# Kernel tuning notes

Hardware: AMD Instinct MI355X
Metric: run time of the kernel (lower is better)

The kernel has to match this reference:

```python
import jax, jax.numpy as jnp
import numpy as np

DIM = 128
HEADS = 8
DIM_HEAD = 128  # must equal DIM for the module's shapes to be consistent
INNER = HEADS * DIM_HEAD  # 1024
B, N = 16, 2048
SCALE = 1.0 / (DIM // 2 + 1)  # 1/65


def setup_inputs() -> dict:
    key = jax.random.key(0)
    k1, k2, k3 = jax.random.split(key, 3)
    x = jax.random.normal(k1, (B, N, DIM), dtype=jnp.float32)
    w_qkv = jax.random.normal(k2, (DIM, 3 * INNER), dtype=jnp.float32) * (DIM ** -0.5)
    w_out = jax.random.normal(k3, (INNER, DIM), dtype=jnp.float32) * (INNER ** -0.5)
    b_out = jnp.zeros((DIM,), dtype=jnp.float32)
    return {"x": x, "w_qkv": w_qkv, "w_out": w_out, "b_out": b_out}


def reference(x, w_qkv, w_out, b_out):
    b, n, dim = x.shape
    qkv = x @ w_qkv                                   # [b, n, 3*inner]
    q, k, v = jnp.split(qkv, 3, axis=-1)
    # b n (h d) -> b h n d
    to_heads = lambda t: t.reshape(b, n, HEADS, DIM_HEAD).transpose(0, 2, 1, 3)
    q, k, v = to_heads(q), to_heads(k), to_heads(v)
    xq_ft = jnp.abs(jnp.fft.rfft(q * SCALE, axis=-1))  # [b, h, n, f] real
    xk_ft = jnp.abs(jnp.fft.rfft(k * SCALE, axis=-1))
    xv_ft = jnp.fft.rfft(v, axis=-1)                   # complex
    att = jnp.einsum('bhex,bhey->bhxy', xq_ft, xk_ft)  # [b, h, f, f]
    att = jax.nn.softmax(att, axis=-1)
    xqkv_ft = jnp.einsum('bhxy,bhey->bhex', att.astype(xv_ft.dtype), xv_ft)
    out = jnp.fft.irfft(xqkv_ft, n=dim, axis=-1)       # [b, h, n, dim]
    out = out.transpose(0, 2, 1, 3).reshape(b, n, HEADS * dim)  # b n (h d)
    return out @ w_out + b_out
```

## Files before the change

kernel.cpp:

```cpp
#include <hip/hip_runtime.h>
#include <hip/hip_bf16.h>
#include <math.h>

#define NB    16
#define NSEQ  2048
#define MROWS (NB*NSEQ)

typedef __attribute__((ext_vector_type(8))) short bf16x8;
typedef __attribute__((ext_vector_type(4))) float f32x4;

__device__ __forceinline__ void g2l16(const void* g, void* l) {
    __builtin_amdgcn_global_load_lds(
        (const __attribute__((address_space(1))) void*)g,
        (__attribute__((address_space(3))) void*)l, 16, 0, 0);
}

__device__ __forceinline__ ushort f2bfu(float x) {
    __hip_bfloat16 t = __float2bfloat16(x);
    return *reinterpret_cast<ushort*>(&t);
}

__global__ __launch_bounds__(256) void k_misc(const float* __restrict__ x,
                                              const float* __restrict__ wqkv,
                                              const float* __restrict__ wout,
                                              __hip_bfloat16* __restrict__ Xb,
                                              ushort* __restrict__ Wvb,
                                              ushort* __restrict__ Wqkb,
                                              ushort* __restrict__ Gcat,
                                              ushort* __restrict__ Fcs,
                                              ushort* __restrict__ Bas) {
    __shared__ float tc[128], ts[128];
    int tid = threadIdx.x;
    int bid = blockIdx.x;
    if (bid < 4096) {
        int i = bid * 256 + tid;
        float4 v = ((const float4*)x)[i];
        __hip_bfloat16 o[4] = {__float2bfloat16(v.x), __float2bfloat16(v.y),
                               __float2bfloat16(v.z), __float2bfloat16(v.w)};
        *(ushort4*)((ushort*)Xb + (size_t)i * 4) = *(const ushort4*)o;
    } else if (bid < 4224) {
        int u = bid - 4096;
        float4 v = *(const float4*)(wqkv + (size_t)u * 3072 + 2048 + tid * 4);
        ushort o[4] = {f2bfu(v.x), f2bfu(v.y), f2bfu(v.z), f2bfu(v.w)};
        *(ushort4*)(Wvb + (size_t)u * 1024 + tid * 4) = *(const ushort4*)o;
    } else if (bid < 4352) {
        int u = bid - 4224;
        #pragma unroll
        for (int it = 0; it < 2; ++it) {
            int i = it * 256 + tid;
            float4 v = ((const float4*)(wqkv + (size_t)u * 3072))[i];
            ushort o[4] = {f2bfu(v.x), f2bfu(v.y), f2bfu(v.z), f2bfu(v.w)};
            *(ushort4*)(Wqkb + (size_t)u * 2048 + i * 4) = *(const ushort4*)o;
        }
    } else if (bid < 4872) {
        int hx = bid - 4352;
        if (tid < 128) {
            float a = (float)tid / 64.0f;
            tc[tid] = cospif(a);
            ts[tid] = sinpif(a);
        }
        __syncthreads();
        if (tid < 128) {
            int h = hx / 65, xx = hx - h * 65;
            float w = (xx == 0 || xx == 64) ? (1.0f / 128.0f) : (2.0f / 128.0f);
            float ar = 0.f, ai = 0.f;
            #pragma unroll 8
            for (int d = 0; d < 128; ++d) {
                float wv = wout[(size_t)(h * 128 + d) * 128 + tid];
                int m = (xx * d) & 127;
                ar = fmaf(wv, tc[m], ar);
                ai = fmaf(wv, ts[m], ai);
            }
            ushort* gp = Gcat + ((size_t)(h * 128 + tid)) * 160;
            gp[xx] = f2bfu(ar * w);
            gp[80 + xx] = f2bfu(-ai * w);
            if (xx == 0) {
                for (int k = 65; k < 80; ++k) gp[k] = 0;
                for (int k = 145; k < 160; ++k) gp[k] = 0;
            }
        }
    } else if (bid < 4888) {
        int r = (bid - 4872) * 16 + (tid >> 4);
        int d = r & 127;
        int y0 = (tid & 15) * 6;
        #pragma unroll
        for (int k = 0; k < 6; ++k) {
            int y = y0 + k;
            float v = 0.f;
            if (y < 65) {
                float a = (float)((d * y) & 127) / 64.0f;
                v = (r < 128) ? cospif(a) : -sinpif(a);
            }
            Fcs[r * 96 + y] = f2bfu(v);
        }
    } else {
        int idx = bid - 4888;
        int rj = idx * 16 + (tid >> 4);
        int ri = (rj >= 80) ? 1 : 0;
        int f = rj - ri * 80;
        int d0 = (tid & 15) * 8;
        #pragma unroll
        for (int k = 0; k < 8; ++k) {
            int d = d0 + k;
            float a = (float)((f * d) & 127) / 64.0f;
            float v = (ri ? -sinpif(a) : cospif(a)) * (1.0f / 65.0f);
            Bas[rj * 128 + d] = f2bfu(v);
        }
    }
}

__global__ __launch_bounds__(256) void k_wfold(const ushort* __restrict__ Wqkb,
                                               const ushort* __restrict__ Bas,
                                               ushort* __restrict__ Wt2) {
    __shared__ ushort As[64 * 128];
    __shared__ ushort Bs[160 * 128];
    int tid = threadIdx.x;
    int wave = tid >> 6, lane = tid & 63;
    int reg = blockIdx.x >> 4;
    int h = (blockIdx.x >> 1) & 7;
    int uh = blockIdx.x & 1;
    const ushort* ga = Wqkb + (size_t)(uh * 64) * 2048 + reg * 1024 + h * 128;
    #pragma unroll
    for (int it = 0; it < 4; ++it) {
        int q0 = wave * 256 + it * 64;
        int q = q0 + lane;
        int row = q >> 4, cp = q & 15;
        int gc = cp ^ (row & 15);
        g2l16(ga + (size_t)row * 2048 + gc * 8, As + q0 * 8);
    }
    #pragma unroll
    for (int it = 0; it < 10; ++it) {
        int q0 = it * 256 + wave * 64;
        int q = q0 + lane;
        int row = q >> 4, cp = q & 15;
        int gc = cp ^ (row & 15);
        g2l16(Bas + (size_t)row * 128 + gc * 8, Bs + q0 * 8);
    }
    __syncthreads();

    f32x4 acc[2][5];
    #pragma unroll
    for (int i = 0; i < 2; ++i)
        #pragma unroll
        for (int j = 0; j < 5; ++j) acc[i][j] = (f32x4){0.f, 0.f, 0.f, 0.f};

    int lr = lane & 15, lk = lane >> 4;
    int wr = (wave >> 1) * 32;
    int wn = (wave & 1) * 80;
    #pragma unroll
    for (int kk = 0; kk < 4; ++kk) {
        bf16x8 af[2], bfr[5];
        int c = kk * 4 + lk;
        #pragma unroll
        for (int i = 0; i < 2; ++i) {
            int m = wr + i * 16 + lr;
            af[i] = *(const bf16x8*)(As + m * 128 + (c ^ (m & 15)) * 8);
        }
        #pragma unroll
        for (int j = 0; j < 5; ++j) {
            int n = wn + j * 16 + lr;
            bfr[j] = *(const bf16x8*)(Bs + n * 128 + (c ^ (n & 15)) * 8);
        }
        #pragma unroll
        for (int i = 0; i < 2; ++i)
            #pragma unroll
            for (int j = 0; j < 5; ++j)
                acc[i][j] = __builtin_amdgcn_mfma_f32_16x16x32_bf16(af[i], bfr[j], acc[i][j], 0, 0, 0);
    }

    #pragma unroll
    for (int j = 0; j < 5; ++j) {
        int rj = wn + j * 16 + lr;
        int n = (h * 2 + reg) * 160 + rj;
        #pragma unroll
        for (int i = 0; i < 2; ++i) {
            int c0 = uh * 64 + wr + i * 16 + lk * 4;
            union { ushort4 u4; ushort u[4]; } pk;
            #pragma unroll
            for (int r = 0; r < 4; ++r) pk.u[r] = f2bfu(acc[i][j][r]);
            *(ushort4*)(Wt2 + (size_t)n * 128 + c0) = pk.u4;
        }
    }
}

__global__ __launch_bounds__(320, 3) void k_fuse(const __hip_bfloat16* __restrict__ Xb,
                                                 const ushort* __restrict__ Wt2,
                                                 float* __restrict__ attp) {
    __shared__ ushort As[128 * 128];
    __shared__ ushort S[160 * 128];
    int tid = threadIdx.x;
    int wave = tid >> 6, lane = tid & 63;
    int lr = lane & 15, lk = lane >> 4;
    int lin = blockIdx.y * 128 + blockIdx.x;
    int nl = (lin & 7) * 64 + (lin >> 3);
    int b = nl >> 5;
    int epart = (nl >> 3) & 3, h = nl & 7;
    size_t erow0 = (size_t)b * NSEQ + (size_t)epart * 512;
    const ushort* wh = Wt2 + (size_t)h * 320 * 128;

    bf16x8 bw[4][4];
    #pragma unroll
    for (int ks = 0; ks < 4; ++ks)
        #pragma unroll
        for (int rb = 0; rb < 4; ++rb) {
            int n = rb * 80 + wave * 16 + lr;
            bw[ks][rb] = *(const bf16x8*)(wh + (size_t)n * 128 + (ks * 4 + lk) * 8);
        }

    {
        const ushort* gx = (const ushort*)Xb + erow0 * 128;
        for (int r = wave; r < 32; r += 5) {
            int q0 = r * 64, q = q0 + lane;
            int row = q >> 4, cp = q & 15;
            int gc = cp ^ (row & 15);
            g2l16(gx + (size_t)row * 128 + gc * 8, As + q0 * 8);
        }
    }
    __syncthreads();

    f32x4 acc2[5];
    #pragma unroll
    for (int j = 0; j < 5; ++j) acc2[j] = (f32x4){0.f, 0.f, 0.f, 0.f};

    for (int it = 0; it < 4; ++it) {
        #pragma unroll
        for (int et = 0; et < 8; ++et) {
            f32x4 a4[4];
            #pragma unroll
            for (int rb = 0; rb < 4; ++rb) a4[rb] = (f32x4){0.f, 0.f, 0.f, 0.f};
            #pragma unroll
            for (int ks = 0; ks < 4; ++ks) {
                int m = et * 16 + lr;
                bf16x8 xa = *(const bf16x8*)(As + m * 128 + (((ks * 4 + lk) ^ (m & 15))) * 8);
                #pragma unroll
                for (int rb = 0; rb < 4; ++rb)
                    a4[rb] = __builtin_amdgcn_mfma_f32_16x16x32_bf16(xa, bw[ks][rb], a4[rb], 0, 0, 0);
            }
            int e4 = et * 16 + lk * 4;
            int cq = e4 >> 3, sub = e4 & 7;
            union { ushort4 u4; ushort u[4]; } pq, pk2;
            #pragma unroll
            for (int r = 0; r < 4; ++r) {
                pq.u[r]  = f2bfu(__builtin_amdgcn_sqrtf(a4[0][r] * a4[0][r] + a4[1][r] * a4[1][r]));
                pk2.u[r] = f2bfu(__builtin_amdgcn_sqrtf(a4[2][r] * a4[2][r] + a4[3][r] * a4[3][r]));
            }
            int fq = wave * 16 + lr;
            int fk = 80 + wave * 16 + lr;
            *(ushort4*)(S + fq * 128 + ((cq ^ (fq & 15)) << 3) + sub) = pq.u4;
            *(ushort4*)(S + fk * 128 + ((cq ^ (fk & 15)) << 3) + sub) = pk2.u4;
        }
        __syncthreads();
        if (it < 3) {
            const ushort* gx = (const ushort*)Xb + (erow0 + (size_t)(it + 1) * 128) * 128;
            for (int r = wave; r < 32; r += 5) {
                int q0 = r * 64, q = q0 + lane;
                int row = q >> 4, cp = q & 15;
                int gc = cp ^ (row & 15);
                g2l16(gx + (size_t)row * 128 + gc * 8, As + q0 * 8);
            }
        }
        #pragma unroll
        for (int ks = 0; ks < 4; ++ks) {
            int cg = ks * 4 + lk;
            int xr = wave * 16 + lr;
            bf16x8 qa = *(const bf16x8*)(S + xr * 128 + ((cg ^ (xr & 15)) << 3));
            #pragma unroll
            for (int kt = 0; kt < 5; ++kt) {
                int yr = 80 + kt * 16 + lr;
                bf16x8 kb = *(const bf16x8*)(S + yr * 128 + ((cg ^ (yr & 15)) << 3));
                acc2[kt] = __builtin_amdgcn_mfma_f32_16x16x32_bf16(qa, kb, acc2[kt], 0, 0, 0);
            }
        }
        __syncthreads();
    }

    float* outp = attp + ((size_t)(b * 8 + h) * 4 + epart) * 6400;
    #pragma unroll
    for (int kt = 0; kt < 5; ++kt)
        #pragma unroll
        for (int r = 0; r < 4; ++r)
            outp[(wave * 16 + lk * 4 + r) * 80 + kt * 16 + lr] = acc2[kt][r];
}

__global__ void k_softmax(const float* __restrict__ attp, ushort* __restrict__ AttB) {
    int xx = blockIdx.x;
    int bh = blockIdx.y;
    int lane = threadIdx.x;
    ushort* Ab = AttB + (size_t)bh * 8320;
    if (xx >= 65) {
        Ab[xx * 104 + lane] = 0;
        if (lane < 40) Ab[xx * 104 + 64 + lane] = 0;
        return;
    }
    const float* base = attp + (size_t)bh * 4 * 6400 + xx * 80;
    float v0 = 0.f, v1 = 0.f;
    #pragma unroll
    for (int c = 0; c < 4; ++c) {
        v0 += base[(size_t)c * 6400 + lane];
        if (lane == 0) v1 += base[(size_t)c * 6400 + 64];
    }
    float v1b = __shfl(v1, 0);
    float m = fmaxf(v0, v1b);
    #pragma unroll
    for (int off = 32; off >= 1; off >>= 1) m = fmaxf(m, __shfl_xor(m, off));
    float e0 = expf(v0 - m);
    float e1 = expf(v1b - m);
    float s = e0;
    #pragma unroll
    for (int off = 32; off >= 1; off >>= 1) s += __shfl_xor(s, off);
    s += e1;
    float inv = 1.0f / s;
    Ab[xx * 104 + lane] = f2bfu(e0 * inv);
    if (lane == 0) Ab[xx * 104 + 64] = f2bfu(e1 * inv);
    if (lane < 39) Ab[xx * 104 + 65 + lane] = 0;
}

__global__ __launch_bounds__(256) void k_TP(const ushort* __restrict__ AttB,
                                            const ushort* __restrict__ Fcs,
                                            const ushort* __restrict__ Gcat,
                                            ushort* __restrict__ Pt) {
    __shared__ ushort A3[128 * 168];
    int tid = threadIdx.x;
    int wave = tid >> 6, lane = tid & 63;
    int lr = lane & 15, quad = lane >> 4;
    int chalf = blockIdx.x, bh = blockIdx.y;
    int b = bh >> 3, h = bh & 7;

    uint2 z2; z2.x = 0; z2.y = 0;
    uint2* A3v = (uint2*)A3;
    #pragma unroll 4
    for (int i = tid; i < 128 * 168 / 4; i += 256) A3v[i] = z2;
    __syncthreads();
    const ushort* Ab = AttB + (size_t)bh * 8320;

    f32x4 acc1[4][5];
    #pragma unroll
    for (int i = 0; i < 4; ++i)
        #pragma unroll
        for (int j = 0; j < 5; ++j) acc1[i][j] = (f32x4){0.f, 0.f, 0.f, 0.f};
    #pragma unroll
    for (int ks = 0; ks < 3; ++ks) {
        bf16x8 af[4], bfr[5];
        #pragma unroll
        for (int mi = 0; mi < 4; ++mi)
            af[mi] = *(const bf16x8*)(Fcs + (size_t)((wave * 4 + mi) * 16 + lr) * 96 + ks * 32 + quad * 8);
        #pragma unroll
        for (int nt = 0; nt < 5; ++nt)
            bfr[nt] = *(const bf16x8*)(Ab + (nt * 16 + lr) * 104 + ks * 32 + quad * 8);
        #pragma unroll
        for (int mi = 0; mi < 4; ++mi)
            #pragma unroll
            for (int nt = 0; nt < 5; ++nt)
                acc1[mi][nt] = __builtin_amdgcn_mfma_f32_16x16x32_bf16(af[mi], bfr[nt], acc1[mi][nt], 0, 0, 0);
    }
    #pragma unroll
    for (int nt = 0; nt < 5; ++nt) {
        int x = nt * 16 + lr;
        if (x < 65) {
            #pragma unroll
            for (int mi = 0; mi < 4; ++mi) {
                int wbase = (wave * 4 + mi) * 16 + quad * 4;
                #pragma unroll
                for (int r = 0; r < 4; ++r) {
                    int which = wbase + r;
                    int d = which & 127;
                    int kc = (which >> 7) * 80 + x;
                    A3[d * 168 + kc] = f2bfu(acc1[mi][nt][r]);
                }
            }
        }
    }
    __syncthreads();

    f32x4 acc2[2][4];
    #pragma unroll
    for (int i = 0; i < 2; ++i)
        #pragma unroll
        for (int j = 0; j < 4; ++j) acc2[i][j] = (f32x4){0.f, 0.f, 0.f, 0.f};
    const ushort* Gh = Gcat + (size_t)h * 128 * 160;
    #pragma unroll
    for (int ks = 0; ks < 5; ++ks) {
        bf16x8 a2[2], b2[4];
        #pragma unroll
        for (int mi = 0; mi < 2; ++mi)
            a2[mi] = *(const bf16x8*)(A3 + ((wave * 2 + mi) * 16 + lr) * 168 + ks * 32 + quad * 8);
        #pragma unroll
        for (int nt = 0; nt < 4; ++nt)
            b2[nt] = *(const bf16x8*)(Gh + (size_t)(chalf * 64 + nt * 16 + lr) * 160 + ks * 32 + quad * 8);
        #pragma unroll
        for (int mi = 0; mi < 2; ++mi)
            #pragma unroll
            for (int nt = 0; nt < 4; ++nt)
                acc2[mi][nt] = __builtin_amdgcn_mfma_f32_16x16x32_bf16(a2[mi], b2[nt], acc2[mi][nt], 0, 0, 0);
    }
    #pragma unroll
    for (int mi = 0; mi < 2; ++mi) {
        int dbase = (wave * 2 + mi) * 16 + quad * 4;
        #pragma unroll
        for (int nt = 0; nt < 4; ++nt) {
            int c = chalf * 64 + nt * 16 + lr;
            union { ushort4 u4; ushort u[4]; } pk;
            #pragma unroll
            for (int r = 0; r < 4; ++r) pk.u[r] = f2bfu(acc2[mi][nt][r]);
            *(ushort4*)(Pt + ((size_t)(b * 128 + c)) * 1024 + h * 128 + dbase) = pk.u4;
        }
    }
}

__global__ __launch_bounds__(256) void k_R(const ushort* __restrict__ Wvb,
                                           const ushort* __restrict__ Pt,
                                           ushort* __restrict__ Rt) {
    __shared__ ushort As[64 * 128];
    __shared__ ushort Bs[64 * 128];
    int tid = threadIdx.x;
    int wave = tid >> 6, lane = tid & 63;
    int b = blockIdx.x >> 2;
    int nq = (blockIdx.x >> 1) & 1;
    int uq = blockIdx.x & 1;
    const ushort* pb = Pt + (size_t)b * 128 * 1024;

    f32x4 acc[2][2];
    #pragma unroll
    for (int i = 0; i < 2; ++i)
        #pragma unroll
        for (int j = 0; j < 2; ++j) acc[i][j] = (f32x4){0.f, 0.f, 0.f, 0.f};

    int lr = lane & 15, lk = lane >> 4;
    int wr = (wave >> 1) * 32, wc = (wave & 1) * 32;

    for (int k0 = 0; k0 < 1024; k0 += 128) {
        __syncthreads();
        #pragma unroll
        for (int it = 0; it < 4; ++it) {
            int q = wave * 256 + it * 64 + lane;
            int row = q >> 4, cp = q & 15;
            int gc = cp ^ (row & 15);
            int lbase = (wave * 256 + it * 64) * 8;
            g2l16(Wvb + (size_t)(uq * 64 + row) * 1024 + k0 + gc * 8, As + lbase);
            g2l16(pb + (size_t)(nq * 64 + row) * 1024 + k0 + gc * 8, Bs + lbase);
        }
        __syncthreads();
        #pragma unroll
        for (int kk = 0; kk < 4; ++kk) {
            bf16x8 af[2], bfr[2];
            int c = kk * 4 + lk;
            #pragma unroll
            for (int i = 0; i < 2; ++i) {
                int m = wr + i * 16 + lr;
                af[i] = *(const bf16x8*)(As + m * 128 + (c ^ (m & 15)) * 8);
                int n = wc + i * 16 + lr;
                bfr[i] = *(const bf16x8*)(Bs + n * 128 + (c ^ (n & 15)) * 8);
            }
            #pragma unroll
            for (int i = 0; i < 2; ++i)
                #pragma unroll
                for (int j = 0; j < 2; ++j)
                    acc[i][j] = __builtin_amdgcn_mfma_f32_16x16x32_bf16(af[i], bfr[j], acc[i][j], 0, 0, 0);
        }
    }
    #pragma unroll
    for (int i = 0; i < 2; ++i) {
        int ubase = uq * 64 + wr + i * 16 + lk * 4;
        #pragma unroll
        for (int j = 0; j < 2; ++j) {
            int n = nq * 64 + wc + j * 16 + lr;
            union { ushort4 u4; ushort u[4]; } pk;
            #pragma unroll
            for (int r = 0; r < 4; ++r) pk.u[r] = f2bfu(acc[i][j][r]);
            *(ushort4*)(Rt + (size_t)b * 16384 + n * 128 + ubase) = pk.u4;
        }
    }
}

__global__ __launch_bounds__(256) void k_out(const __hip_bfloat16* __restrict__ Xb,
                                             const ushort* __restrict__ Rt,
                                             const float* __restrict__ bout,
                                             float* __restrict__ out) {
    __shared__ ushort As[128 * 128];
    __shared__ ushort Bs[128 * 128];
    int tid = threadIdx.x;
    int wave = tid >> 6, lane = tid & 63;
    int m0 = blockIdx.x * 128;
    int b = blockIdx.x >> 4;
    const ushort* ga = (const ushort*)Xb + (size_t)m0 * 128;
    const ushort* gb = Rt + (size_t)b * 16384;
    #pragma unroll
    for (int it = 0; it < 8; ++it) {
        int q = wave * 512 + it * 64 + lane;
        int row = q >> 4, cp = q & 15;
        int gc = cp ^ (row & 15);
        int lbase = (wave * 512 + it * 64) * 8;
        g2l16(ga + (size_t)row * 128 + gc * 8, As + lbase);
        g2l16(gb + (size_t)row * 128 + gc * 8, Bs + lbase);
    }
    __syncthreads();

    f32x4 acc[4][4];
    #pragma unroll
    for (int i = 0; i < 4; ++i)
        #pragma unroll
        for (int j = 0; j < 4; ++j) acc[i][j] = (f32x4){0.f, 0.f, 0.f, 0.f};

    int lr = lane & 15, lk = lane >> 4;
    int wr = (wave >> 1) * 64, wc = (wave & 1) * 64;
    #pragma unroll
    for (int kk = 0; kk < 4; ++kk) {
        bf16x8 af[4], bfr[4];
        int c = kk * 4 + lk;
        #pragma unroll
        for (int i = 0; i < 4; ++i) {
            int m = wr + i * 16 + lr;
            af[i] = *(const bf16x8*)(As + m * 128 + (c ^ (m & 15)) * 8);
            int n = wc + i * 16 + lr;
            bfr[i] = *(const bf16x8*)(Bs + n * 128 + (c ^ (n & 15)) * 8);
        }
        #pragma unroll
        for (int i = 0; i < 4; ++i)
            #pragma unroll
            for (int j = 0; j < 4; ++j)
                acc[i][j] = __builtin_amdgcn_mfma_f32_16x16x32_bf16(af[i], bfr[j], acc[i][j], 0, 0, 0);
    }

    #pragma unroll
    for (int i = 0; i < 4; ++i) {
        int gr = m0 + wr + i * 16 + lk * 4;
        #pragma unroll
        for (int j = 0; j < 4; ++j) {
            int gcol = wc + j * 16 + lr;
            float bias = bout[gcol];
            #pragma unroll
            for (int r = 0; r < 4; ++r)
                out[(size_t)(gr + r) * 128 + gcol] = acc[i][j][r] + bias;
        }
    }
}

extern "C" void kernel_launch(void* const* d_in, const int* in_sizes, int n_in,
                              void* d_out, int out_size, void* d_ws, size_t ws_size,
                              hipStream_t stream) {
    const float* x    = (const float*)d_in[0];
    const float* wqkv = (const float*)d_in[1];
    const float* wout = (const float*)d_in[2];
    const float* bout = (const float*)d_in[3];
    float* out = (float*)d_out;

    char* ws = (char*)d_ws;
    size_t off = 0;
    auto alloc = [&](size_t bytes) -> void* {
        void* p = (void*)(ws + off);
        off += (bytes + 255) & ~(size_t)255;
        return p;
    };
    ushort* Wt2  = (ushort*)alloc((size_t)8 * 320 * 128 * 2);
    ushort* Gcat = (ushort*)alloc((size_t)8 * 128 * 160 * 2);
    ushort* Fcs  = (ushort*)alloc((size_t)256 * 96 * 2);
    ushort* Wvb  = (ushort*)alloc((size_t)128 * 1024 * 2);
    ushort* Wqkb = (ushort*)alloc((size_t)128 * 2048 * 2);
    ushort* Bas  = (ushort*)alloc((size_t)160 * 128 * 2);
    __hip_bfloat16* Xb = (__hip_bfloat16*)alloc((size_t)MROWS * 128 * 2);
    float* attp = (float*)alloc((size_t)128 * 4 * 6400 * 4);
    ushort* AttB = (ushort*)alloc((size_t)128 * 8320 * 2);
    ushort* Pt  = (ushort*)alloc((size_t)16 * 128 * 1024 * 2);
    ushort* Rt  = (ushort*)alloc((size_t)16 * 128 * 128 * 2);

    k_misc<<<dim3(4898), 256, 0, stream>>>(x, wqkv, wout, Xb, Wvb, Wqkb, Gcat, Fcs, Bas);
    k_wfold<<<dim3(32), 256, 0, stream>>>(Wqkb, Bas, Wt2);
    k_fuse<<<dim3(128, 4), 320, 0, stream>>>(Xb, Wt2, attp);
    k_softmax<<<dim3(80, 128), 64, 0, stream>>>(attp, AttB);
    k_TP<<<dim3(2, 128), 256, 0, stream>>>(AttB, Fcs, Gcat, Pt);
    k_R<<<dim3(64), 256, 0, stream>>>(Wvb, Pt, Rt);
    k_out<<<dim3(256), 256, 0, stream>>>(Xb, Rt, bout, out);
}
```

Measured before the change: 148.4 us.

## Split k_fuse work across 10 waves, halving per-wave Q/K and attention tiles

Doubles the k_fuse block from 5 to 10 waves. Each wave pair now splits the projection work: one wave computes the Q magnitude rows and the other the K magnitude rows. The attention-score tiles are split 3/2 between the two waves. This halves per-wave register use and MFMA chains so more waves can hide latency, at the cost of an uneven split in the attention phase and a lower blocks-per-CU bound.

```diff
diff --git a/kernel.cpp b/kernel.cpp
--- a/kernel.cpp
+++ b/kernel.cpp
@@ -183,7 +183,7 @@
     }
 }
 
-__global__ __launch_bounds__(320, 3) void k_fuse(const __hip_bfloat16* __restrict__ Xb,
+__global__ __launch_bounds__(640, 2) void k_fuse(const __hip_bfloat16* __restrict__ Xb,
                                                  const ushort* __restrict__ Wt2,
                                                  float* __restrict__ attp) {
     __shared__ ushort As[128 * 128];
@@ -191,6 +191,8 @@
     int tid = threadIdx.x;
     int wave = tid >> 6, lane = tid & 63;
     int lr = lane & 15, lk = lane >> 4;
+    int g = wave >> 1;
+    int half = wave & 1;
     int lin = blockIdx.y * 128 + blockIdx.x;
     int nl = (lin & 7) * 64 + (lin >> 3);
     int b = nl >> 5;
@@ -198,18 +200,18 @@
     size_t erow0 = (size_t)b * NSEQ + (size_t)epart * 512;
     const ushort* wh = Wt2 + (size_t)h * 320 * 128;
 
-    bf16x8 bw[4][4];
+    bf16x8 bw[4][2];
     #pragma unroll
     for (int ks = 0; ks < 4; ++ks)
         #pragma unroll
-        for (int rb = 0; rb < 4; ++rb) {
-            int n = rb * 80 + wave * 16 + lr;
-            bw[ks][rb] = *(const bf16x8*)(wh + (size_t)n * 128 + (ks * 4 + lk) * 8);
+        for (int j = 0; j < 2; ++j) {
+            int n = (half * 2 + j) * 80 + g * 16 + lr;
+            bw[ks][j] = *(const bf16x8*)(wh + (size_t)n * 128 + (ks * 4 + lk) * 8);
         }
 
     {
         const ushort* gx = (const ushort*)Xb + erow0 * 128;
-        for (int r = wave; r < 32; r += 5) {
+        for (int r = wave; r < 32; r += 10) {
             int q0 = r * 64, q = q0 + lane;
             int row = q >> 4, cp = q & 15;
             int gc = cp ^ (row & 15);
@@ -218,41 +220,40 @@
     }
     __syncthreads();
 
-    f32x4 acc2[5];
-    #pragma unroll
-    for (int j = 0; j < 5; ++j) acc2[j] = (f32x4){0.f, 0.f, 0.f, 0.f};
+    f32x4 acc2[3];
+    #pragma unroll
+    for (int j = 0; j < 3; ++j) acc2[j] = (f32x4){0.f, 0.f, 0.f, 0.f};
+
+    int srow = half * 80 + g * 16 + lr;
+    int sw = (srow & 15);
+    int ktb = half * 3;
+    int nkt = half ? 2 : 3;
 
     for (int it = 0; it < 4; ++it) {
         #pragma unroll
         for (int et = 0; et < 8; ++et) {
-            f32x4 a4[4];
-            #pragma unroll
-            for (int rb = 0; rb < 4; ++rb) a4[rb] = (f32x4){0.f, 0.f, 0.f, 0.f};
+            f32x4 a2[2];
+            a2[0] = (f32x4){0.f, 0.f, 0.f, 0.f};
+            a2[1] = (f32x4){0.f, 0.f, 0.f, 0.f};
             #pragma unroll
             for (int ks = 0; ks < 4; ++ks) {
                 int m = et * 16 + lr;
                 bf16x8 xa = *(const bf16x8*)(As + m * 128 + (((ks * 4 + lk) ^ (m & 15))) * 8);
-                #pragma unroll
-                for (int rb = 0; rb < 4; ++rb)
-                    a4[rb] = __builtin_amdgcn_mfma_f32_16x16x32_bf16(xa, bw[ks][rb], a4[rb], 0, 0, 0);
+                a2[0] = __builtin_amdgcn_mfma_f32_16x16x32_bf16(xa, bw[ks][0], a2[0], 0, 0, 0);
+                a2[1] = __builtin_amdgcn_mfma_f32_16x16x32_bf16(xa, bw[ks][1], a2[1], 0, 0, 0);
             }
             int e4 = et * 16 + lk * 4;
             int cq = e4 >> 3, sub = e4 & 7;
-            union { ushort4 u4; ushort u[4]; } pq, pk2;
-            #pragma unroll
-            for (int r = 0; r < 4; ++r) {
-                pq.u[r]  = f2bfu(__builtin_amdgcn_sqrtf(a4[0][r] * a4[0][r] + a4[1][r] * a4[1][r]));
-                pk2.u[r] = f2bfu(__builtin_amdgcn_sqrtf(a4[2][r] * a4[2][r] + a4[3][r] * a4[3][r]));
-            }
-            int fq = wave * 16 + lr;
-            int fk = 80 + wave * 16 + lr;
-            *(ushort4*)(S + fq * 128 + ((cq ^ (fq & 15)) << 3) + sub) = pq.u4;
-            *(ushort4*)(S + fk * 128 + ((cq ^ (fk & 15)) << 3) + sub) = pk2.u4;
+            union { ushort4 u4; ushort u[4]; } pm;
+            #pragma unroll
+            for (int r = 0; r < 4; ++r)
+                pm.u[r] = f2bfu(__builtin_amdgcn_sqrtf(a2[0][r] * a2[0][r] + a2[1][r] * a2[1][r]));
+            *(ushort4*)(S + srow * 128 + ((cq ^ sw) << 3) + sub) = pm.u4;
         }
         __syncthreads();
         if (it < 3) {
             const ushort* gx = (const ushort*)Xb + (erow0 + (size_t)(it + 1) * 128) * 128;
-            for (int r = wave; r < 32; r += 5) {
+            for (int r = wave; r < 32; r += 10) {
                 int q0 = r * 64, q = q0 + lane;
                 int row = q >> 4, cp = q & 15;
                 int gc = cp ^ (row & 15);
@@ -262,13 +263,16 @@
         #pragma unroll
         for (int ks = 0; ks < 4; ++ks) {
             int cg = ks * 4 + lk;
-            int xr = wave * 16 + lr;
+            int xr = g * 16 + lr;
             bf16x8 qa = *(const bf16x8*)(S + xr * 128 + ((cg ^ (xr & 15)) << 3));
             #pragma unroll
-            for (int kt = 0; kt < 5; ++kt) {
-                int yr = 80 + kt * 16 + lr;
-                bf16x8 kb = *(const bf16x8*)(S + yr * 128 + ((cg ^ (yr & 15)) << 3));
-                acc2[kt] = __builtin_amdgcn_mfma_f32_16x16x32_bf16(qa, kb, acc2[kt], 0, 0, 0);
+            for (int j = 0; j < 3; ++j) {
+                if (j < nkt) {
+                    int kt = ktb + j;
+                    int yr = 80 + kt * 16 + lr;
+                    bf16x8 kb = *(const bf16x8*)(S + yr * 128 + ((cg ^ (yr & 15)) << 3));
+                    acc2[j] = __builtin_amdgcn_mfma_f32_16x16x32_bf16(qa, kb, acc2[j], 0, 0, 0);
+                }
             }
         }
         __syncthreads();
@@ -276,10 +280,14 @@
 
     float* outp = attp + ((size_t)(b * 8 + h) * 4 + epart) * 6400;
     #pragma unroll
-    for (int kt = 0; kt < 5; ++kt)
-        #pragma unroll
-        for (int r = 0; r < 4; ++r)
-            outp[(wave * 16 + lk * 4 + r) * 80 + kt * 16 + lr] = acc2[kt][r];
+    for (int j = 0; j < 3; ++j) {
+        if (j < nkt) {
+            int kt = ktb + j;
+            #pragma unroll
+            for (int r = 0; r < 4; ++r)
+                outp[(g * 16 + lk * 4 + r) * 80 + kt * 16 + lr] = acc2[j][r];
+        }
+    }
 }
 
 __global__ void k_softmax(const float* __restrict__ attp, ushort* __restrict__ AttB) {
@@ -565,7 +573,7 @@
 
     k_misc<<<dim3(4898), 256, 0, stream>>>(x, wqkv, wout, Xb, Wvb, Wqkb, Gcat, Fcs, Bas);
     k_wfold<<<dim3(32), 256, 0, stream>>>(Wqkb, Bas, Wt2);
-    k_fuse<<<dim3(128, 4), 320, 0, stream>>>(Xb, Wt2, attp);
+    k_fuse<<<dim3(128, 4), 640, 0, stream>>>(Xb, Wt2, attp);
     k_softmax<<<dim3(80, 128), 64, 0, stream>>>(attp, AttB);
     k_TP<<<dim3(2, 128), 256, 0, stream>>>(AttB, Fcs, Gcat, Pt);
     k_R<<<dim3(64), 256, 0, stream>>>(Wvb, Pt, Rt);
```

After: 140.4 us (median of 2 runs). 1.06x faster.
